# Optimization experiments

Hardware: AMD Instinct MI355X
Metric: run time of the kernel (lower is better)

## Reference

```python
import jax, jax.numpy as jnp
import numpy as np

FILTER_SIZE = 3   # window length
MAJORITY = 2      # min ones per window -> at most one zero per window of 3
BIG = 1e30        # finite 'infinity' (fp32-safe)


def _segment_masks(target):
    """Precompute (from the integer target, a constant) per-timestep masks.
    Returns [T,B] float32 masks: is_zero, forced_one, dp_active, seg_start, seg_end.
    Runs of ones shorter than FILTER_SIZE are forced all-ones (len<majority, or
    len==2 with f=min(3,2)=2,m=2 -> both ones). Runs with len>=3 use the window DP."""
    t = np.asarray(target).astype(bool)
    B, T = t.shape
    prev = np.concatenate([np.zeros((B, 1), bool), t[:, :-1]], axis=1)
    nxt = np.concatenate([t[:, 1:], np.zeros((B, 1), bool)], axis=1)
    starts = t & ~prev
    ends = t & ~nxt
    idx = np.broadcast_to(np.arange(T)[None, :], (B, T))
    sidx = np.maximum.accumulate(np.where(starts, idx, -1), axis=1)
    eidx = np.minimum.accumulate(np.where(ends, idx, T)[:, ::-1], axis=1)[:, ::-1]
    run_len = np.where(t, eidx - sidx + 1, 0)
    forced = t & (run_len < FILTER_SIZE)
    dp_act = t & (run_len >= FILTER_SIZE)
    f32 = lambda a: jnp.asarray(np.ascontiguousarray(a.T), dtype=jnp.float32)
    return f32(~t), f32(forced), f32(dp_act), f32(dp_act & starts), f32(dp_act & ends)


def _median_filter_loss(c0, c1, mz, mf, ma, ms, me):
    """c0/c1: [B,T] losses vs target 0/1. Masks [T,B]. DP state = last two bits
    (index 2*prev2 + prev1); window constraint: every 3-window has >=2 ones,
    equivalently transitions: new[0]=inf; new[1]=dp[2]+c1; new[2]=dp[3]+c0;
    new[3]=min(dp[1],dp[3])+c1. Segment start resets to state (1,1) cost 0
    (ones-padding adds no extra constraints for f=3,m=2)."""
    B = c0.shape[0]
    reset = jnp.array([BIG, BIG, BIG, 0.0], c0.dtype)

    def step(carry, x):
        dp, loss = carry
        c0t, c1t, mzt, mft, mat, mst, met = x
        dpi = jnp.where(mst[:, None] > 0, reset[None, :], dp)
        n1 = dpi[:, 2] + c1t
        n2 = dpi[:, 3] + c0t
        n3 = jnp.minimum(dpi[:, 1], dpi[:, 3]) + c1t
        tr = jnp.stack([jnp.full((B,), BIG, c0t.dtype), n1, n2, n3], axis=1)
        tr = jnp.minimum(tr, BIG)
        dpn = jnp.where(mat[:, None] > 0, tr, dp)
        seg_min = jnp.min(dpn, axis=1)  # finite at segment ends (all-ones path valid)
        loss = loss + jnp.sum(mzt * c0t + mft * c1t + met * seg_min)
        return (dpn, loss), None

    xs = (c0.T, c1.T, mz, mf, ma, ms, me)
    dp0 = jnp.full((B, 4), BIG, c0.dtype).at[:, 3].set(0.0)
    (_, loss), _ = jax.lax.scan(step, (dp0, jnp.zeros((), c0.dtype)), xs)
    return loss


def setup_inputs() -> dict:
    key = jax.random.key(0)
    k1, k2 = jax.random.split(key)
    output = jax.random.normal(k1, (1024, 16384), dtype=jnp.float32)
    target = jax.random.randint(k2, (1024, 16384), 0, 2, dtype=jnp.int32)
    return {"output": output, "target": target}


def reference(output, target):
    # BCEWithLogitsLoss(reduction='none'): vs zeros -> softplus(x); vs ones -> softplus(-x)
    c0 = jax.nn.softplus(output)
    c1 = jax.nn.softplus(-output)
    mz, mf, ma, ms, me = _segment_masks(target)
    loss = _median_filter_loss(c0, c1, mz, mf, ma, ms, me)
    return loss / output.size  # reduction='mean'
```

## Files before the change

### kernel.cpp

```cpp
#include <hip/hip_runtime.h>

#define T_LEN 16384
#define K_CHUNK 32
#define BIGF 1e30f

__device__ __forceinline__ void sp_pair(float xv, float& c0, float& c1) {
    float e = __expf(-fabsf(xv));
    float l = __logf(1.0f + e);
    c1 = fmaxf(-xv, 0.0f) + l;
    c0 = c1 + xv;
}

__global__ void mfl_zero(float* out) {
    if (threadIdx.x == 0) out[0] = 0.0f;
}

__global__ __launch_bounds__(256) void mfl_main(const float* __restrict__ x,
                                                const int* __restrict__ tgt,
                                                float* __restrict__ res,
                                                int total, float inv_total) {
    const int nchunks = total / K_CHUNK;
    const int stride = gridDim.x * blockDim.x;
    float acc = 0.0f;

    for (int c = blockIdx.x * blockDim.x + threadIdx.x; c < nchunks; c += stride) {
        const int p0 = c * K_CHUNK;
        const int trow = p0 & (T_LEN - 1);

        float xs[32];
        unsigned m = 0;
        const float4* xp = (const float4*)(x + p0);
        const int4*  tp = (const int4*)(tgt + p0);
        #pragma unroll
        for (int j = 0; j < 8; j++) {
            float4 v = xp[j];
            xs[4*j+0] = v.x; xs[4*j+1] = v.y; xs[4*j+2] = v.z; xs[4*j+3] = v.w;
        }
        #pragma unroll
        for (int j = 0; j < 8; j++) {
            int4 t = tp[j];
            m |= (unsigned)(t.x != 0) << (4*j+0);
            m |= (unsigned)(t.y != 0) << (4*j+1);
            m |= (unsigned)(t.z != 0) << (4*j+2);
            m |= (unsigned)(t.w != 0) << (4*j+3);
        }

        unsigned amask = 0xFFFFFFFFu;
        if (trow != 0 && tgt[p0 - 1] != 0) {
            unsigned nm = ~m;
            amask = (nm == 0u) ? 0u : (0xFFFFFFFFu << __builtin_ctz(nm));
        }
        const unsigned mm = m & amask;
        const unsigned zm = (~m) & amask;

        float v1 = BIGF, v2 = BIGF, v3 = 0.0f, s1 = 0.0f;
        int   leni = 0;
        unsigned prev = 0;
        #pragma unroll
        for (int i = 0; i < 32; i++) {
            float c0, c1;
            sp_pair(xs[i], c0, c1);
            const unsigned one = (mm >> i) & 1u;
            const unsigned za  = (zm >> i) & 1u;
            const bool endf = (prev & (one ^ 1u)) != 0u;
            const float hv = (leni < 3) ? s1 : fminf(v1, fminf(v2, v3));
            acc += endf ? hv : 0.0f;
            acc += za ? c0 : 0.0f;
            const bool startf = (one & (prev ^ 1u)) != 0u;
            const float r1 = startf ? BIGF : v1;
            const float r2 = startf ? BIGF : v2;
            const float r3 = startf ? 0.0f : v3;
            s1   = startf ? 0.0f : s1;
            leni = startf ? 0    : leni;
            v1 = r2 + c1;
            v2 = r3 + c0;
            v3 = fminf(r1, r3) + c1;
            s1 += c1;
            leni += 1;
            prev = one;
        }

        if (prev) {
            int t = trow + K_CHUNK, pp = p0 + K_CHUNK;
            while (t < T_LEN) {
                const int4   tq = *(const int4*)(tgt + pp);
                const float4 xq = *(const float4*)(x + pp);
                const unsigned g = (unsigned)(tq.x != 0)
                                 | ((unsigned)(tq.y != 0) << 1)
                                 | ((unsigned)(tq.z != 0) << 2)
                                 | ((unsigned)(tq.w != 0) << 3);
                const int k = (g == 0xFu) ? 4 : (int)__builtin_ctz(~g & 0xFu);
                const float xv[4] = {xq.x, xq.y, xq.z, xq.w};
                #pragma unroll
                for (int j = 0; j < 4; j++) {
                    if (j < k) {
                        float c0, c1;
                        sp_pair(xv[j], c0, c1);
                        const float n1 = v2 + c1;
                        const float n2 = v3 + c0;
                        const float n3 = fminf(v1, v3) + c1;
                        v1 = n1; v2 = n2; v3 = n3;
                        s1 += c1; leni++;
                    }
                }
                if (k < 4) break;
                t += 4; pp += 4;
            }
            acc += (leni < 3) ? s1 : fminf(v1, fminf(v2, v3));
        }
    }

    #pragma unroll
    for (int off = 32; off > 0; off >>= 1)
        acc += __shfl_down(acc, off);

    __shared__ float smem[4];
    const int lane = threadIdx.x & 63;
    const int wid = threadIdx.x >> 6;
    if (lane == 0) smem[wid] = acc;
    __syncthreads();
    if (threadIdx.x == 0) {
        float b = (smem[0] + smem[1]) + (smem[2] + smem[3]);
        atomicAdd(res, b * inv_total);
    }
}

extern "C" void kernel_launch(void* const* d_in, const int* in_sizes, int n_in,
                              void* d_out, int out_size, void* d_ws, size_t ws_size,
                              hipStream_t stream) {
    const float* x = (const float*)d_in[0];
    const int* tgt = (const int*)d_in[1];
    float* res = (float*)d_out;
    const int total = in_sizes[0];

    mfl_zero<<<1, 64, 0, stream>>>(res);

    const int threads = 256;
    const int nchunks = total / K_CHUNK;
    const int blocks = (nchunks + threads - 1) / threads;
    mfl_main<<<blocks, threads, 0, stream>>>(x, tgt, res, total,
                                             1.0f / (float)total);
}
```

Baseline: 159.6 us.

## Rebase DP costs on softplus(x) and preload lookahead tail for runs

Uses c1 = c0 - x to compute only one softplus per element, which is always added to the accumulator. The DP transitions are shifted to subtract x instead of adding c1 and c0, so per-step transcendentals drop from one softplus pair to a single softplus. Run start and end masks are now computed with bit tricks, and the next 8 elements are prefetched unconditionally so runs that spill past a chunk usually finish without a dependent serial loop. In exchange there are extra loads for every chunk and possible floating-point reassociation differences.

```diff
diff --git a/kernel.cpp b/kernel.cpp
--- a/kernel.cpp
+++ b/kernel.cpp
@@ -4,11 +4,10 @@
 #define K_CHUNK 32
 #define BIGF 1e30f
 
-__device__ __forceinline__ void sp_pair(float xv, float& c0, float& c1) {
+__device__ __forceinline__ float sp0(float xv) {
     float e = __expf(-fabsf(xv));
     float l = __logf(1.0f + e);
-    c1 = fmaxf(-xv, 0.0f) + l;
-    c0 = c1 + xv;
+    return fmaxf(xv, 0.0f) + l;
 }
 
 __global__ void mfl_zero(float* out) {
@@ -45,66 +44,94 @@
             m |= (unsigned)(t.w != 0) << (4*j+3);
         }
 
+        const int pl = (p0 + K_CHUNK + 8 <= total) ? (p0 + K_CHUNK) : p0;
+        float la[8];
+        unsigned lm = 0;
+        {
+            const float4* lxp = (const float4*)(x + pl);
+            const int4*  ltp = (const int4*)(tgt + pl);
+            float4 a0 = lxp[0], a1 = lxp[1];
+            int4   b0 = ltp[0], b1 = ltp[1];
+            la[0]=a0.x; la[1]=a0.y; la[2]=a0.z; la[3]=a0.w;
+            la[4]=a1.x; la[5]=a1.y; la[6]=a1.z; la[7]=a1.w;
+            lm  = (unsigned)(b0.x!=0)      | ((unsigned)(b0.y!=0)<<1)
+                | ((unsigned)(b0.z!=0)<<2) | ((unsigned)(b0.w!=0)<<3)
+                | ((unsigned)(b1.x!=0)<<4) | ((unsigned)(b1.y!=0)<<5)
+                | ((unsigned)(b1.z!=0)<<6) | ((unsigned)(b1.w!=0)<<7);
+        }
+
         unsigned amask = 0xFFFFFFFFu;
         if (trow != 0 && tgt[p0 - 1] != 0) {
             unsigned nm = ~m;
             amask = (nm == 0u) ? 0u : (0xFFFFFFFFu << __builtin_ctz(nm));
         }
         const unsigned mm = m & amask;
-        const unsigned zm = (~m) & amask;
+        const unsigned ss = mm & ~(mm << 1);
+        const unsigned hm = (~mm) & (mm << 1);
 
         float v1 = BIGF, v2 = BIGF, v3 = 0.0f, s1 = 0.0f;
-        int   leni = 0;
-        unsigned prev = 0;
+        int leni = 0;
         #pragma unroll
         for (int i = 0; i < 32; i++) {
-            float c0, c1;
-            sp_pair(xs[i], c0, c1);
-            const unsigned one = (mm >> i) & 1u;
-            const unsigned za  = (zm >> i) & 1u;
-            const bool endf = (prev & (one ^ 1u)) != 0u;
+            const float xv = xs[i];
+            acc += sp0(xv);
+            const bool harvf = (hm >> i) & 1u;
             const float hv = (leni < 3) ? s1 : fminf(v1, fminf(v2, v3));
-            acc += endf ? hv : 0.0f;
-            acc += za ? c0 : 0.0f;
-            const bool startf = (one & (prev ^ 1u)) != 0u;
+            acc += harvf ? hv : 0.0f;
+            const bool startf = (ss >> i) & 1u;
             const float r1 = startf ? BIGF : v1;
             const float r2 = startf ? BIGF : v2;
             const float r3 = startf ? 0.0f : v3;
-            s1   = startf ? 0.0f : s1;
-            leni = startf ? 0    : leni;
-            v1 = r2 + c1;
-            v2 = r3 + c0;
-            v3 = fminf(r1, r3) + c1;
-            s1 += c1;
-            leni += 1;
-            prev = one;
+            const float s1r = startf ? 0.0f : s1;
+            const int   lr  = startf ? 0    : leni;
+            v1 = r2 - xv;
+            v2 = r3;
+            v3 = fminf(r1, r3) - xv;
+            s1 = s1r - xv;
+            leni = lr + 1;
         }
 
-        if (prev) {
-            int t = trow + K_CHUNK, pp = p0 + K_CHUNK;
-            while (t < T_LEN) {
-                const int4   tq = *(const int4*)(tgt + pp);
-                const float4 xq = *(const float4*)(x + pp);
-                const unsigned g = (unsigned)(tq.x != 0)
-                                 | ((unsigned)(tq.y != 0) << 1)
-                                 | ((unsigned)(tq.z != 0) << 2)
-                                 | ((unsigned)(tq.w != 0) << 3);
-                const int k = (g == 0xFu) ? 4 : (int)__builtin_ctz(~g & 0xFu);
-                const float xv[4] = {xq.x, xq.y, xq.z, xq.w};
+        if ((mm >> 31) & 1u) {
+            if (trow + K_CHUNK < T_LEN) {
+                const unsigned g = lm & 0xFFu;
+                const int k = (g == 0xFFu) ? 8 : (int)__builtin_ctz(~g & 0xFFu);
                 #pragma unroll
-                for (int j = 0; j < 4; j++) {
+                for (int j = 0; j < 8; j++) {
                     if (j < k) {
-                        float c0, c1;
-                        sp_pair(xv[j], c0, c1);
-                        const float n1 = v2 + c1;
-                        const float n2 = v3 + c0;
-                        const float n3 = fminf(v1, v3) + c1;
+                        const float xv = la[j];
+                        const float n1 = v2 - xv;
+                        const float n2 = v3;
+                        const float n3 = fminf(v1, v3) - xv;
                         v1 = n1; v2 = n2; v3 = n3;
-                        s1 += c1; leni++;
+                        s1 -= xv; leni++;
                     }
                 }
-                if (k < 4) break;
-                t += 4; pp += 4;
+                if (k == 8) {
+                    int t = trow + K_CHUNK + 8, pp = p0 + K_CHUNK + 8;
+                    while (t < T_LEN) {
+                        const int4   tq = *(const int4*)(tgt + pp);
+                        const float4 xq = *(const float4*)(x + pp);
+                        const unsigned g4 = (unsigned)(tq.x != 0)
+                                          | ((unsigned)(tq.y != 0) << 1)
+                                          | ((unsigned)(tq.z != 0) << 2)
+                                          | ((unsigned)(tq.w != 0) << 3);
+                        const int k4 = (g4 == 0xFu) ? 4 : (int)__builtin_ctz(~g4 & 0xFu);
+                        const float xv4[4] = {xq.x, xq.y, xq.z, xq.w};
+                        #pragma unroll
+                        for (int j = 0; j < 4; j++) {
+                            if (j < k4) {
+                                const float xv = xv4[j];
+                                const float n1 = v2 - xv;
+                                const float n2 = v3;
+                                const float n3 = fminf(v1, v3) - xv;
+                                v1 = n1; v2 = n2; v3 = n3;
+                                s1 -= xv; leni++;
+                            }
+                        }
+                        if (k4 < 4) break;
+                        t += 4; pp += 4;
+                    }
+                }
             }
             acc += (leni < 3) ? s1 : fminf(v1, fminf(v2, v3));
         }
```

New measurement: 155.4 us. 2.7% less time.
